# Kernel optimization log

Measured on AMD Instinct MI355X. Metric: run time of the kernel, lower is better.

Reference implementation:

```python
import jax, jax.numpy as jnp
import numpy as np

SEG = 512        # seg_len
REUSE = 2        # reuse_seg_num
D = 512          # d_model
K = 512          # k_dim
NL = 6           # layers per encoder
NSEG = 8         # number of segments (context 4096)
VOCAB = 10000
FF = 2048
MEM = REUSE * SEG


def sinusoid_pos_encode(length, dim):
    pos = jnp.arange(length, dtype=jnp.float32)[:, None]
    idx = jnp.arange(0, dim, 2, dtype=jnp.float32)
    ang = pos / jnp.power(10000.0, idx / dim)
    pe = jnp.zeros((length, dim), dtype=jnp.float32)
    pe = pe.at[:, 0::2].set(jnp.sin(ang))
    pe = pe.at[:, 1::2].set(jnp.cos(ang))
    return pe


def layernorm(x, g, b, eps=1e-5):
    mu = jnp.mean(x, axis=-1, keepdims=True)
    var = jnp.mean(jnp.square(x - mu), axis=-1, keepdims=True)
    return (x - mu) * jax.lax.rsqrt(var + eps) * g + b


def run_encoder(tokens, emb, Wqkvr, Wo, W1, W2, ln, uv):
    # tokens: (NSEG*SEG,) int
    segs = tokens.reshape(NSEG, SEG)
    R = jnp.flip(sinusoid_pos_encode(MEM + SEG, K), axis=0)  # flipped rel. encoding
    u, v = uv[0], uv[1]                                       # (K,), (K,)
    scale = 1.0 / np.sqrt(K)

    def step(prev, xs):
        seg, seg_idx = xs
        state = emb[seg]                                      # (SEG, D)
        # memory validity mask: only the last min(seg_idx, REUSE) segments are real
        n_valid = jnp.minimum(seg_idx, REUSE) * SEG
        mem_bias = jnp.where(jnp.arange(MEM) >= MEM - n_valid, 0.0, -1e9)
        bias = jnp.concatenate([mem_bias, jnp.zeros(SEG)])    # (MEM+SEG,)
        recs = []
        for j in range(NL):
            recs.append(state)
            mem = prev[:, j].reshape(MEM, D)                  # (MEM, D)
            Wq, Wk, Wv, Wr = Wqkvr[j]                         # each (D, K)
            q = state @ Wq                                    # (SEG, K)
            full = jnp.concatenate([mem, state], axis=0)      # (MEM+SEG, D)
            k = full @ Wk
            val = full @ Wv
            pk = R @ Wr                                       # (MEM+SEG, K)
            scores = ((q + u) @ k.T + (q + v) @ pk.T) * scale + bias[None, :]
            attn = jax.nn.softmax(scores, axis=-1)            # (SEG, MEM+SEG)
            out = (attn @ val) @ Wo[j]                        # (SEG, D)
            h = layernorm(state + out, ln[j, 0], ln[j, 1])
            ff = jax.nn.relu(h @ W1[j]) @ W2[j]
            state = layernorm(h + ff, ln[j, 2], ln[j, 3])
        # shift memory: drop oldest, append pre-layer states of this segment
        prev_new = jnp.concatenate([prev[1:], jnp.stack(recs)[None]], axis=0)
        return prev_new, state

    prev0 = jnp.zeros((REUSE, NL, SEG, D), dtype=jnp.float32)
    _, outs = jax.lax.scan(step, prev0, (segs, jnp.arange(NSEG)))
    return outs.reshape(-1, D)  # (NSEG*SEG, D)


def setup_inputs() -> dict:
    key = jax.random.key(0)
    ks = jax.random.split(key, 16)
    s = 0.02
    def mk(k, shape):
        return jax.random.normal(k, shape, dtype=jnp.float32) * s
    inp = {
        "src": jax.random.randint(ks[0], (1, NSEG * SEG), 0, VOCAB, dtype=jnp.int32),
        "pad_idx": 0,
        "emb": mk(ks[1], (VOCAB, D)),
        "Wqkvr_a": mk(ks[2], (NL, 4, D, K)),
        "Wo_a": mk(ks[3], (NL, K, D)),
        "W1_a": mk(ks[4], (NL, D, FF)),
        "W2_a": mk(ks[5], (NL, FF, D)),
        "ln_a": jnp.tile(jnp.array([1.0, 0.0, 1.0, 0.0], dtype=jnp.float32)[None, :, None], (NL, 1, D)),
        "uv_a": jax.random.normal(ks[6], (2, K), dtype=jnp.float32),
        "Wqkvr_b": mk(ks[7], (NL, 4, D, K)),
        "Wo_b": mk(ks[8], (NL, K, D)),
        "W1_b": mk(ks[9], (NL, D, FF)),
        "W2_b": mk(ks[10], (NL, FF, D)),
        "ln_b": jnp.tile(jnp.array([1.0, 0.0, 1.0, 0.0], dtype=jnp.float32)[None, :, None], (NL, 1, D)),
        "uv_b": jax.random.normal(ks[11], (2, K), dtype=jnp.float32),
    }
    return inp


def reference(src, pad_idx, emb, Wqkvr_a, Wo_a, W1_a, W2_a, ln_a, uv_a,
              Wqkvr_b, Wo_b, W1_b, W2_b, ln_b, uv_b):
    tokens = src[0]
    fwd = run_encoder(tokens, emb, Wqkvr_a, Wo_a, W1_a, W2_a, ln_a, uv_a)
    rev = run_encoder(tokens[::-1], emb, Wqkvr_b, Wo_b, W1_b, W2_b, ln_b, uv_b)
    rev = rev[::-1]
    return jnp.concatenate([fwd, rev], axis=-1)  # (NSEG*SEG, 2*D)
```

## Files before the change

kernel.cpp:

```cpp
#include <hip/hip_runtime.h>

typedef __bf16 bf16;
typedef __bf16 bf16x8 __attribute__((ext_vector_type(8)));
typedef __bf16 bf16x4 __attribute__((ext_vector_type(4)));
typedef __bf16 bf16x2 __attribute__((ext_vector_type(2)));
typedef float f32x4 __attribute__((ext_vector_type(4)));

typedef __attribute__((address_space(3))) void lds_void_t;
typedef const __attribute__((address_space(1))) void gbl_void_t;

#define TOK 4096
#define KBROWS 5120

enum { M_BF16 = 0, M_F32 = 1, M_RELU = 2, M_QKV = 3, M_SCOREXP = 4, M_PV = 5 };

struct GemmArgs {
  const bf16* A; long long sAe, sAi; int ldA;
  const bf16* B; long long sBe, sBi; int ldB;
  const bf16* B2; long long sB2e; int ldB2;
  bf16* C; float* Cf; long long sCe, sCi; int ldC;
  int M, N, K, iPerE;
  bf16 *quv, *kbuf, *vt;
  const float *uvA, *uvB;
  float scale;
};

template<int MODE, bool SPLITB, int TM, int TN>
__global__ __launch_bounds__(256, 4)
void gemm_kernel(GemmArgs g) {
  constexpr int FA = TM / 32, FB = TN / 32;
  int z = blockIdx.z;
  int e = z / g.iPerE;
  int i = z % g.iPerE;
  const bf16* A = g.A + e * g.sAe + i * g.sAi;
  const bf16* B = g.B + e * g.sBe + i * g.sBi;
  const bf16* B2 = nullptr;
  if constexpr (SPLITB) B2 = g.B2 + e * g.sB2e;

  int tm = blockIdx.x * TM;
  int tn = blockIdx.y * TN;

  __shared__ uint4 As4[TM * 8];
  __shared__ uint4 Bs4[TN * 8];
  __shared__ float ls[MODE == M_PV ? TM : 1];
  bf16* As_lds = (bf16*)As4;
  bf16* Bs_lds = (bf16*)Bs4;

  int tid = threadIdx.x;
  int wave = tid >> 6, lane = tid & 63;
  int wm = (wave >> 1) * (TM / 2), wn = (wave & 1) * (TN / 2);
  int quad = lane >> 4, l15 = lane & 15;
  int l7 = l15 & 7;
  int l8r = lane >> 3, l8c = lane & 7;
  int fc = l8c ^ l8r;

  f32x4 acc[FA][FB] = {};
  float lreg[FA];
#pragma unroll
  for (int t = 0; t < FA; ++t) lreg[t] = 0.f;

  for (int k0 = 0; k0 < g.K; k0 += 64) {
#pragma unroll
    for (int ii = 0; ii < FA; ++ii) {
      int rowbase = (wave * FA + ii) * 8;
      int r = rowbase + l8r;
      const bf16* gp = &A[(long long)(tm + r) * g.ldA + k0 + fc * 8];
      __builtin_amdgcn_global_load_lds((gbl_void_t*)gp, (lds_void_t*)&As_lds[rowbase * 64], 16, 0, 0);
    }
#pragma unroll
    for (int ii = 0; ii < FB; ++ii) {
      int rowbase = (wave * FB + ii) * 8;
      int r = rowbase + l8r;
      const bf16* gp;
      if constexpr (SPLITB) {
        int kk = k0 + fc * 8;
        gp = (kk < 512) ? &B[(long long)(tn + r) * g.ldB + kk]
                        : &B2[(long long)(tn + r) * g.ldB2 + (kk - 512)];
      } else {
        gp = &B[(long long)(tn + r) * g.ldB + k0 + fc * 8];
      }
      __builtin_amdgcn_global_load_lds((gbl_void_t*)gp, (lds_void_t*)&Bs_lds[rowbase * 64], 16, 0, 0);
    }
    __syncthreads();
#pragma unroll
    for (int s = 0; s < 2; ++s) {
      int sw = (s * 4 + quad) ^ l7;
      bf16x8 af[FA], bfr[FB];
#pragma unroll
      for (int t = 0; t < FA; ++t) af[t]  = ((const bf16x8*)As4)[(wm + t * 16 + l15) * 8 + sw];
#pragma unroll
      for (int t = 0; t < FB; ++t) bfr[t] = ((const bf16x8*)Bs4)[(wn + t * 16 + l15) * 8 + sw];
      if constexpr (MODE == M_PV) {
#pragma unroll
        for (int t = 0; t < FA; ++t)
#pragma unroll
          for (int q2 = 0; q2 < 8; ++q2) lreg[t] += (float)af[t][q2];
      }
#pragma unroll
      for (int a = 0; a < FA; ++a)
#pragma unroll
        for (int b = 0; b < FB; ++b)
          acc[a][b] = __builtin_amdgcn_mfma_f32_16x16x32_bf16(af[a], bfr[b], acc[a][b], 0, 0, 0);
    }
    __syncthreads();
  }

  if constexpr (MODE == M_PV) {
#pragma unroll
    for (int t = 0; t < FA; ++t) {
      lreg[t] += __shfl_xor(lreg[t], 16);
      lreg[t] += __shfl_xor(lreg[t], 32);
      if (quad == 0) ls[wm + t * 16 + l15] = lreg[t];
    }
    __syncthreads();
  }

  if constexpr (MODE == M_QKV) {
    const float* uv = e ? g.uvB : g.uvA;
#pragma unroll
    for (int a = 0; a < FA; ++a) {
      int mB = tm + wm + a * 16 + quad * 4;
#pragma unroll
      for (int b = 0; b < FB; ++b) {
        int col = tn + wn + b * 16 + l15;
        int region = col >> 9, cin = col & 511;
        float u0 = 0.f, v0 = 0.f;
        if (region == 0) { u0 = uv[cin]; v0 = uv[512 + cin]; }
#pragma unroll
        for (int r = 0; r < 4; ++r) {
          int m = mB + r;
          float val = acc[a][b][r];
          if (region == 0) {
            long long qb = (long long)e * TOK * 1024 + (long long)m * 1024;
            g.quv[qb + cin]       = (bf16)(val + u0);
            g.quv[qb + 512 + cin] = (bf16)(val + v0);
          } else if (region == 1) {
            g.kbuf[(long long)e * KBROWS * 512 + (long long)(1024 + m) * 512 + cin] = (bf16)val;
          } else {
            g.vt[(long long)e * 512 * KBROWS + (long long)cin * KBROWS + 1024 + m] = (bf16)val;
          }
        }
      }
    }
  } else if constexpr (MODE == M_SCOREXP) {
    bf16* C = g.C + e * g.sCe + i * g.sCi;
    int T = 1024 - ((i < 2 ? i : 2) << 9);
#pragma unroll
    for (int a = 0; a < FA; ++a) {
      int mB = tm + wm + a * 16 + quad * 4;
#pragma unroll
      for (int b = 0; b < FB; ++b) {
        int col = tn + wn + b * 16 + l15;
        float bias = (col < T) ? -1e9f : 0.0f;
#pragma unroll
        for (int r = 0; r < 4; ++r)
          C[(long long)(mB + r) * g.ldC + col] = (bf16)__expf(acc[a][b][r] * g.scale + bias);
      }
    }
  } else if constexpr (MODE == M_PV) {
    float* Cf = g.Cf + e * g.sCe + i * g.sCi;
#pragma unroll
    for (int a = 0; a < FA; ++a) {
      int lrow = wm + a * 16 + quad * 4;
      int mB = tm + lrow;
#pragma unroll
      for (int b = 0; b < FB; ++b) {
        int col = tn + wn + b * 16 + l15;
#pragma unroll
        for (int r = 0; r < 4; ++r)
          Cf[(long long)(mB + r) * g.ldC + col] = acc[a][b][r] / ls[lrow + r];
      }
    }
  } else {
#pragma unroll
    for (int a = 0; a < FA; ++a) {
      int mB = tm + wm + a * 16 + quad * 4;
#pragma unroll
      for (int b = 0; b < FB; ++b) {
        int col = tn + wn + b * 16 + l15;
#pragma unroll
        for (int r = 0; r < 4; ++r) {
          float val = acc[a][b][r];
          if constexpr (MODE == M_RELU) val = val > 0.f ? val : 0.f;
          if constexpr (MODE == M_F32) {
            float* Cf = g.Cf + e * g.sCe + i * g.sCi;
            Cf[(long long)(mB + r) * g.ldC + col] = val;
          } else {
            bf16* C = g.C + e * g.sCe + i * g.sCi;
            C[(long long)(mB + r) * g.ldC + col] = (bf16)val;
          }
        }
      }
    }
  }
}

__device__ inline void prep_locate(int id, const float* qa, const float* qb,
                                   const float* oa, const float* ob,
                                   const float* w1a, const float* w1b,
                                   const float* w2a, const float* w2b,
                                   bf16* wqkvT, bf16* wrT, bf16* wvPlain, bf16* woT,
                                   bf16* w1T, bf16* w2T,
                                   const float*& src, bf16*& dst, int& R, int& C,
                                   int& tx, int& ty, bool& plain) {
  plain = false;
  if (id < 3072) {
    int mat = id >> 6, tile = id & 63;
    tx = tile & 7; ty = tile >> 3;
    int e = mat / 24, rj = mat % 24, j = rj >> 2, c = rj & 3;
    src = (e ? qb : qa) + (long long)(j * 4 + c) * 262144;
    R = 512; C = 512;
    if (c < 2)        dst = wqkvT + ((long long)(e * 6 + j) * 3 + c) * 262144;
    else if (c == 2) { dst = wvPlain + (long long)(e * 6 + j) * 262144; plain = true; }
    else              dst = wrT + (long long)(e * 6 + j) * 262144;
  } else if (id < 3840) {
    int id2 = id - 3072; int mat = id2 >> 6, tile = id2 & 63;
    tx = tile & 7; ty = tile >> 3;
    int e = mat / 6, j = mat % 6;
    src = (e ? ob : oa) + (long long)j * 262144;
    dst = woT + (long long)mat * 262144; R = 512; C = 512;
  } else if (id < 6912) {
    int id2 = id - 3840; int mat = id2 >> 8, tile = id2 & 255;
    tx = tile & 31; ty = tile >> 5;
    int e = mat / 6, j = mat % 6;
    src = (e ? w1b : w1a) + (long long)j * 512 * 2048;
    dst = w1T + (long long)mat * 512 * 2048; R = 512; C = 2048;
  } else {
    int id2 = id - 6912; int mat = id2 >> 8, tile = id2 & 255;
    tx = tile & 7; ty = tile >> 3;
    int e = mat / 6, j = mat % 6;
    src = (e ? w2b : w2a) + (long long)j * 2048 * 512;
    dst = w2T + (long long)mat * 2048 * 512; R = 2048; C = 512;
  }
}

__global__ __launch_bounds__(256)
void prep_weights(const float* qa, const float* qb, const float* oa, const float* ob,
                  const float* w1a, const float* w1b, const float* w2a, const float* w2b,
                  bf16* wqkvT, bf16* wrT, bf16* wvPlain, bf16* woT, bf16* w1T, bf16* w2T) {
  int id0 = blockIdx.x * 2;
  const float* src; bf16* dst; int R, C, tx0, ty; bool plain;
  prep_locate(id0, qa, qb, oa, ob, w1a, w1b, w2a, w2b,
              wqkvT, wrT, wvPlain, woT, w1T, w2T, src, dst, R, C, tx0, ty, plain);
  int r0 = ty * 64;
  int tid = threadIdx.x;

  if (plain) {
    int c8 = (tid & 7) * 8;
    int r8 = tid >> 3;
    float4 f[2][4];
#pragma unroll
    for (int p = 0; p < 2; ++p) {
      int c0 = (tx0 + p) * 64;
#pragma unroll
      for (int rep = 0; rep < 2; ++rep) {
        const float* sp = &src[(long long)(r0 + r8 + rep * 32) * C + c0 + c8];
        f[p][rep * 2]     = *(const float4*)sp;
        f[p][rep * 2 + 1] = *(const float4*)(sp + 4);
      }
    }
#pragma unroll
    for (int p = 0; p < 2; ++p) {
      int c0 = (tx0 + p) * 64;
#pragma unroll
      for (int rep = 0; rep < 2; ++rep) {
        float4 f0 = f[p][rep * 2], f1 = f[p][rep * 2 + 1];
        bf16 o[8] __attribute__((aligned(16))) =
          {(bf16)f0.x, (bf16)f0.y, (bf16)f0.z, (bf16)f0.w,
           (bf16)f1.x, (bf16)f1.y, (bf16)f1.z, (bf16)f1.w};
        *(bf16x8*)&dst[(long long)(r0 + r8 + rep * 32) * C + c0 + c8] = *(const bf16x8*)o;
      }
    }
  } else {
    __shared__ bf16 t[2][64 * 68];
    int l15 = tid & 15;
    int hi  = tid >> 4;
    int cc = l15 * 4;
    float4 f[2][4];
#pragma unroll
    for (int p = 0; p < 2; ++p) {
      int c0 = (tx0 + p) * 64;
#pragma unroll
      for (int rep = 0; rep < 4; ++rep)
        f[p][rep] = *(const float4*)&src[(long long)(r0 + hi + rep * 16) * C + c0 + cc];
    }
#pragma unroll
    for (int p = 0; p < 2; ++p)
#pragma unroll
      for (int rep = 0; rep < 4; ++rep) {
        int rr = hi + rep * 16;
        float v[4] = {f[p][rep].x, f[p][rep].y, f[p][rep].z, f[p][rep].w};
#pragma unroll
        for (int i2 = 0; i2 < 4; ++i2) {
          int row = cc + i2;
          int col = rr ^ (((row >> 4) & 3) << 2);
          t[p][row * 68 + col] = (bf16)v[i2];
        }
      }
    __syncthreads();
    int oc = tid >> 2;
    int kk = tid & 3;
#pragma unroll
    for (int p = 0; p < 2; ++p) {
      int c0 = (tx0 + p) * 64;
      bf16 outv[16] __attribute__((aligned(16)));
#pragma unroll
      for (int u = 0; u < 4; ++u) {
        int col = (16 * kk + 4 * u) ^ (((oc >> 4) & 3) << 2);
        *(bf16x4*)&outv[u * 4] = *(const bf16x4*)&t[p][oc * 68 + col];
      }
      bf16* dp = &dst[(long long)(c0 + oc) * R + r0 + 16 * kk];
      *(bf16x8*)dp       = *(const bf16x8*)&outv[0];
      *(bf16x8*)(dp + 8) = *(const bf16x8*)&outv[8];
    }
  }
}

__global__ __launch_bounds__(256)
void sinusoid_kernel(bf16* rb) {
  int i = blockIdx.x, m = threadIdx.x;
  float p = (float)(1535 - i);
  float inv = expf(-((float)(2 * m) * (1.0f / 512.0f)) * 9.210340371976184f);
  float ang = p * inv;
  bf16x2 v = {(bf16)sinf(ang), (bf16)cosf(ang)};
  *(bf16x2*)&rb[(long long)i * 512 + 2 * m] = v;
}

__global__ __launch_bounds__(128)
void embed_kernel(const int* src, const float* emb, bf16* Sb, float* Sf) {
  int row = blockIdx.x, e = blockIdx.y, tid = threadIdx.x;
  int tok = e ? src[4095 - row] : src[row];
  long long base = ((long long)e * TOK + row) * 512 + tid * 4;
  float4 f = *(const float4*)&emb[(long long)tok * 512 + tid * 4];
  *(float4*)&Sf[base] = f;
  bf16 o[4] __attribute__((aligned(8))) = {(bf16)f.x, (bf16)f.y, (bf16)f.z, (bf16)f.w};
  *(bf16x4*)&Sb[base] = *(const bf16x4*)o;
}

__global__ __launch_bounds__(256)
void zero_kv(bf16* kbuf, bf16* vwoT) {
  int r = blockIdx.x, e = blockIdx.y, which = blockIdx.z, tid = threadIdx.x;
  uint4 z = {0u, 0u, 0u, 0u};
  if (which == 0) {
    if (tid < 64) ((uint4*)(kbuf + ((long long)e * KBROWS + r) * 512))[tid] = z;
  } else if (r < 512) {
    if (tid < 128) ((uint4*)(vwoT + ((long long)e * 512 + r) * KBROWS))[tid] = z;
  }
}

__global__ __launch_bounds__(64)
void ln_kernel(const float* Xf, const float* Tf, const float* lnA, const float* lnB,
               int gOff, bf16* OutB, float* OutF, int outMode, float* finalOut) {
  int row = blockIdx.x, e = blockIdx.y;
  long long base = ((long long)e * TOK + row) * 512;
  const float* ln = e ? lnB : lnA;
  int lane = threadIdx.x;
  int d0 = lane * 8;
  float4 x0 = *(const float4*)&Xf[base + d0];
  float4 x1 = *(const float4*)&Xf[base + d0 + 4];
  float4 t0 = *(const float4*)&Tf[base + d0];
  float4 t1 = *(const float4*)&Tf[base + d0 + 4];
  float vals[8] = {x0.x + t0.x, x0.y + t0.y, x0.z + t0.z, x0.w + t0.w,
                   x1.x + t1.x, x1.y + t1.y, x1.z + t1.z, x1.w + t1.w};
  float s = 0.f;
#pragma unroll
  for (int k = 0; k < 8; ++k) s += vals[k];
  for (int off = 32; off; off >>= 1) s += __shfl_xor(s, off);
  float mu = s * (1.0f / 512.0f);
  float vs = 0.f;
#pragma unroll
  for (int k = 0; k < 8; ++k) { float d = vals[k] - mu; vs += d * d; }
  for (int off = 32; off; off >>= 1) vs += __shfl_xor(vs, off);
  float rstd = rsqrtf(vs * (1.0f / 512.0f) + 1e-5f);
  float4 g0 = *(const float4*)&ln[gOff + d0];
  float4 g1 = *(const float4*)&ln[gOff + d0 + 4];
  float4 b0 = *(const float4*)&ln[gOff + 512 + d0];
  float4 b1 = *(const float4*)&ln[gOff + 512 + d0 + 4];
  float gm[8] = {g0.x, g0.y, g0.z, g0.w, g1.x, g1.y, g1.z, g1.w};
  float bt[8] = {b0.x, b0.y, b0.z, b0.w, b1.x, b1.y, b1.z, b1.w};
  float y[8];
#pragma unroll
  for (int k = 0; k < 8; ++k) y[k] = (vals[k] - mu) * rstd * gm[k] + bt[k];
  if (outMode == 0) {
    bf16 ob8[8] __attribute__((aligned(16)));
#pragma unroll
    for (int k = 0; k < 8; ++k) ob8[k] = (bf16)y[k];
    *(bf16x8*)&OutB[base + d0] = *(const bf16x8*)ob8;
    float4 ya = {y[0], y[1], y[2], y[3]}, yb = {y[4], y[5], y[6], y[7]};
    *(float4*)&OutF[base + d0]     = ya;
    *(float4*)&OutF[base + d0 + 4] = yb;
  } else {
    long long ob = e ? ((long long)(4095 - row) * 1024 + 512) : ((long long)row * 1024);
    float4 ya = {y[0], y[1], y[2], y[3]}, yb = {y[4], y[5], y[6], y[7]};
    *(float4*)&finalOut[ob + d0]     = ya;
    *(float4*)&finalOut[ob + d0 + 4] = yb;
  }
}

extern "C" void kernel_launch(void* const* d_in, const int* in_sizes, int n_in,
                              void* d_out, int out_size, void* d_ws, size_t ws_size,
                              hipStream_t stream) {
  const int*   src   = (const int*)d_in[0];
  const float* emb   = (const float*)d_in[2];
  const float* Wq_a  = (const float*)d_in[3];
  const float* Wo_a  = (const float*)d_in[4];
  const float* W1_a  = (const float*)d_in[5];
  const float* W2_a  = (const float*)d_in[6];
  const float* ln_a  = (const float*)d_in[7];
  const float* uv_a  = (const float*)d_in[8];
  const float* Wq_b  = (const float*)d_in[9];
  const float* Wo_b  = (const float*)d_in[10];
  const float* W1_b  = (const float*)d_in[11];
  const float* W2_b  = (const float*)d_in[12];
  const float* ln_b  = (const float*)d_in[13];
  const float* uv_b  = (const float*)d_in[14];
  float* out = (float*)d_out;

  char* w = (char*)d_ws;
  size_t off = 0;
  auto alloc = [&](long long elems, int esz) -> char* {
    char* p = w + off;
    off += (size_t)elems * esz;
    off = (off + 255) & ~(size_t)255;
    return p;
  };
  bf16* wqkvT = (bf16*)alloc(2LL * 6 * 1536 * 512, 2);
  bf16* woT   = (bf16*)alloc(2LL * 6 * 512 * 512, 2);
  bf16* w1T   = (bf16*)alloc(2LL * 6 * 2048 * 512, 2);
  bf16* w2T   = (bf16*)alloc(2LL * 6 * 512 * 2048, 2);
  bf16* pk    = (bf16*)alloc(2LL * 6 * 1536 * 512, 2);
  bf16* Sb    = (bf16*)alloc(2LL * TOK * 512, 2);
  float* Sf   = (float*)alloc(2LL * TOK * 512, 4);
  bf16* quv   = (bf16*)alloc(2LL * TOK * 1024, 2);
  bf16* kbuf  = (bf16*)alloc(2LL * KBROWS * 512, 2);
  bf16* vwoT  = (bf16*)alloc(2LL * 512 * KBROWS, 2);
  bf16* P     = (bf16*)alloc(2LL * 8 * 512 * 1536, 2);
  float* t1f  = (float*)alloc(2LL * TOK * 512, 4);
  bf16* f1    = (bf16*)alloc(2LL * TOK * 2048, 2);
  bf16* rb      = f1;
  bf16* wrT     = f1 + 1024LL * 1024;
  bf16* wvPlain = f1 + 4096LL * 1024;

  if (off > ws_size) return;

  prep_weights<<<4992, 256, 0, stream>>>(Wq_a, Wq_b, Wo_a, Wo_b, W1_a, W1_b, W2_a, W2_b,
                                         wqkvT, wrT, wvPlain, woT, w1T, w2T);
  sinusoid_kernel<<<1536, 256, 0, stream>>>(rb);
  embed_kernel<<<dim3(4096, 2), 128, 0, stream>>>(src, emb, Sb, Sf);
  zero_kv<<<dim3(1024, 2, 2), 256, 0, stream>>>(kbuf, vwoT);

  {
    GemmArgs g = {};
    g.A = rb; g.sAe = 0; g.sAi = 0; g.ldA = 512;
    g.B = wrT; g.sBe = 0; g.sBi = 512LL * 512; g.ldB = 512;
    g.C = pk; g.sCe = 0; g.sCi = 1536LL * 512; g.ldC = 512;
    g.M = 1536; g.N = 512; g.K = 512; g.iPerE = 12;
    gemm_kernel<M_BF16, false, 128, 128><<<dim3(12, 4, 12), 256, 0, stream>>>(g);
  }
  {
    GemmArgs g = {};
    g.A = woT; g.sAe = 6LL * 262144; g.sAi = 262144; g.ldA = 512;
    g.B = wvPlain; g.sBe = 6LL * 262144; g.sBi = 262144; g.ldB = 512;
    g.C = wqkvT + 2LL * 262144; g.sCe = 18LL * 262144; g.sCi = 3LL * 262144; g.ldC = 512;
    g.M = 512; g.N = 512; g.K = 512; g.iPerE = 6;
    gemm_kernel<M_BF16, false, 128, 128><<<dim3(4, 4, 12), 256, 0, stream>>>(g);
  }

  const float scale = 0.044194173824159216f;

  for (int j = 0; j < 6; ++j) {
    {
      GemmArgs g = {};
      g.A = Sb; g.sAe = (long long)TOK * 512; g.sAi = 0; g.ldA = 512;
      g.B = wqkvT + (long long)j * 1536 * 512; g.sBe = 6LL * 1536 * 512; g.sBi = 0; g.ldB = 512;
      g.M = TOK; g.N = 1536; g.K = 512; g.iPerE = 1;
      g.quv = quv; g.kbuf = kbuf; g.vt = vwoT; g.uvA = uv_a; g.uvB = uv_b;
      gemm_kernel<M_QKV, false, 128, 128><<<dim3(32, 12, 2), 256, 0, stream>>>(g);
    }
    {
      GemmArgs g = {};
      g.A = quv; g.sAe = (long long)TOK * 1024; g.sAi = 512LL * 1024; g.ldA = 1024;
      g.B = kbuf; g.sBe = (long long)KBROWS * 512; g.sBi = 512LL * 512; g.ldB = 512;
      g.B2 = pk + (long long)j * 1536 * 512; g.sB2e = 6LL * 1536 * 512; g.ldB2 = 512;
      g.C = P; g.sCe = 8LL * 512 * 1536; g.sCi = 512LL * 1536; g.ldC = 1536;
      g.M = 512; g.N = 1536; g.K = 1024; g.iPerE = 8;
      g.scale = scale;
      gemm_kernel<M_SCOREXP, true, 128, 128><<<dim3(4, 12, 16), 256, 0, stream>>>(g);
    }
    {
      GemmArgs g = {};
      g.A = P; g.sAe = 8LL * 512 * 1536; g.sAi = 512LL * 1536; g.ldA = 1536;
      g.B = vwoT; g.sBe = 512LL * KBROWS; g.sBi = 512; g.ldB = KBROWS;
      g.Cf = t1f; g.sCe = (long long)TOK * 512; g.sCi = 512LL * 512; g.ldC = 512;
      g.M = 512; g.N = 512; g.K = 1536; g.iPerE = 8;
      gemm_kernel<M_PV, false, 64, 128><<<dim3(8, 4, 16), 256, 0, stream>>>(g);
    }
    ln_kernel<<<dim3(4096, 2), 64, 0, stream>>>(Sf, t1f, ln_a, ln_b, (j * 4 + 0) * 512, Sb, Sf, 0, out);
    {
      GemmArgs g = {};
      g.A = Sb; g.sAe = (long long)TOK * 512; g.sAi = 0; g.ldA = 512;
      g.B = w1T + (long long)j * 2048 * 512; g.sBe = 6LL * 2048 * 512; g.sBi = 0; g.ldB = 512;
      g.C = f1; g.sCe = (long long)TOK * 2048; g.sCi = 0; g.ldC = 2048;
      g.M = TOK; g.N = 2048; g.K = 512; g.iPerE = 1;
      gemm_kernel<M_RELU, false, 128, 128><<<dim3(32, 16, 2), 256, 0, stream>>>(g);
    }
    {
      GemmArgs g = {};
      g.A = f1; g.sAe = (long long)TOK * 2048; g.sAi = 0; g.ldA = 2048;
      g.B = w2T + (long long)j * 512 * 2048; g.sBe = 6LL * 512 * 2048; g.sBi = 0; g.ldB = 2048;
      g.Cf = t1f; g.sCe = (long long)TOK * 512; g.sCi = 0; g.ldC = 512;
      g.M = TOK; g.N = 512; g.K = 2048; g.iPerE = 1;
      gemm_kernel<M_F32, false, 64, 128><<<dim3(64, 4, 2), 256, 0, stream>>>(g);
    }
    ln_kernel<<<dim3(4096, 2), 64, 0, stream>>>(Sf, t1f, ln_a, ln_b, (j * 4 + 2) * 512, Sb, Sf,
                                                (j == 5) ? 1 : 0, out);
  }
}
```

Measured before the change: 1.275 ms.

## Fuse setup kernels into one launch and stage V-transpose stores through LDS

Merges weight prep, sinusoid generation, embedding lookup and KV zeroing into one setup kernel, with each weight-prep block now handling four tiles instead of two. In the QKV GEMM epilogue the region is resolved per tile rather than per element, and the V-transposed output is staged through shared memory so it is written with 16-byte coalesced stores instead of scattered 2-byte strided writes. This is meant to cut launch overhead and uncoalesced global writes. The cost is more register pressure in the prep path and extra LDS traffic and a barrier in the epilogue.

Result: faster. 1.243 ms (-2.5%).

```diff
diff --git a/kernel.cpp b/kernel.cpp
--- a/kernel.cpp
+++ b/kernel.cpp
@@ -40,8 +40,9 @@
   int tm = blockIdx.x * TM;
   int tn = blockIdx.y * TN;
 
-  __shared__ uint4 As4[TM * 8];
-  __shared__ uint4 Bs4[TN * 8];
+  __shared__ uint4 smem[TM * 8 + TN * 8];
+  uint4* As4 = smem;
+  uint4* Bs4 = smem + TM * 8;
   __shared__ float ls[MODE == M_PV ? TM : 1];
   bf16* As_lds = (bf16*)As4;
   bf16* Bs_lds = (bf16*)Bs4;
@@ -117,28 +118,61 @@
 
   if constexpr (MODE == M_QKV) {
     const float* uv = e ? g.uvB : g.uvA;
-#pragma unroll
-    for (int a = 0; a < FA; ++a) {
-      int mB = tm + wm + a * 16 + quad * 4;
-#pragma unroll
-      for (int b = 0; b < FB; ++b) {
-        int col = tn + wn + b * 16 + l15;
-        int region = col >> 9, cin = col & 511;
-        float u0 = 0.f, v0 = 0.f;
-        if (region == 0) { u0 = uv[cin]; v0 = uv[512 + cin]; }
-#pragma unroll
-        for (int r = 0; r < 4; ++r) {
-          int m = mB + r;
-          float val = acc[a][b][r];
-          if (region == 0) {
+    int region = tn >> 9;
+    if (region == 2) {
+      bf16* sm = (bf16*)smem;
+#pragma unroll
+      for (int a = 0; a < FA; ++a) {
+        int m_l = wm + a * 16 + quad * 4;
+#pragma unroll
+        for (int b = 0; b < FB; ++b) {
+          int c_l = wn + b * 16 + l15;
+          int mp = m_l ^ ((c_l & 15) << 3);
+          bf16 v4[4] __attribute__((aligned(8)));
+#pragma unroll
+          for (int r = 0; r < 4; ++r) v4[r] = (bf16)acc[a][b][r];
+          *(bf16x4*)&sm[c_l * 128 + mp] = *(const bf16x4*)v4;
+        }
+      }
+      __syncthreads();
+      int c_l = tid >> 1;
+      int half = (tid & 1) * 64;
+      long long vb = (long long)e * 512 * KBROWS + (long long)(tn - 1024 + c_l) * KBROWS + 1024 + tm;
+#pragma unroll
+      for (int u = 0; u < 8; ++u) {
+        int m0 = half + u * 8;
+        int mp = m0 ^ ((c_l & 15) << 3);
+        *(bf16x8*)&g.vt[vb + m0] = *(const bf16x8*)&sm[c_l * 128 + mp];
+      }
+    } else if (region == 0) {
+#pragma unroll
+      for (int a = 0; a < FA; ++a) {
+        int mB = tm + wm + a * 16 + quad * 4;
+#pragma unroll
+        for (int b = 0; b < FB; ++b) {
+          int cin = tn + wn + b * 16 + l15;
+          float u0 = uv[cin], v0 = uv[512 + cin];
+#pragma unroll
+          for (int r = 0; r < 4; ++r) {
+            int m = mB + r;
+            float val = acc[a][b][r];
             long long qb = (long long)e * TOK * 1024 + (long long)m * 1024;
             g.quv[qb + cin]       = (bf16)(val + u0);
             g.quv[qb + 512 + cin] = (bf16)(val + v0);
-          } else if (region == 1) {
-            g.kbuf[(long long)e * KBROWS * 512 + (long long)(1024 + m) * 512 + cin] = (bf16)val;
-          } else {
-            g.vt[(long long)e * 512 * KBROWS + (long long)cin * KBROWS + 1024 + m] = (bf16)val;
           }
+        }
+      }
+    } else {
+#pragma unroll
+      for (int a = 0; a < FA; ++a) {
+        int mB = tm + wm + a * 16 + quad * 4;
+#pragma unroll
+        for (int b = 0; b < FB; ++b) {
+          int cin = (tn - 512) + wn + b * 16 + l15;
+#pragma unroll
+          for (int r = 0; r < 4; ++r)
+            g.kbuf[(long long)e * KBROWS * 512 + (long long)(1024 + mB + r) * 512 + cin] =
+                (bf16)acc[a][b][r];
         }
       }
     }
@@ -235,116 +269,151 @@
 }
 
 __global__ __launch_bounds__(256)
-void prep_weights(const float* qa, const float* qb, const float* oa, const float* ob,
+void setup_kernel(const float* qa, const float* qb, const float* oa, const float* ob,
                   const float* w1a, const float* w1b, const float* w2a, const float* w2b,
-                  bf16* wqkvT, bf16* wrT, bf16* wvPlain, bf16* woT, bf16* w1T, bf16* w2T) {
-  int id0 = blockIdx.x * 2;
-  const float* src; bf16* dst; int R, C, tx0, ty; bool plain;
-  prep_locate(id0, qa, qb, oa, ob, w1a, w1b, w2a, w2b,
-              wqkvT, wrT, wvPlain, woT, w1T, w2T, src, dst, R, C, tx0, ty, plain);
-  int r0 = ty * 64;
+                  bf16* wqkvT, bf16* wrT, bf16* wvPlain, bf16* woT, bf16* w1T, bf16* w2T,
+                  bf16* rb, const int* src, const float* emb, bf16* Sb, float* Sf,
+                  bf16* kbuf, bf16* vwoT) {
+  __shared__ bf16 t[2][64 * 68];
+  int bid = blockIdx.x;
   int tid = threadIdx.x;
 
-  if (plain) {
-    int c8 = (tid & 7) * 8;
-    int r8 = tid >> 3;
-    float4 f[2][4];
-#pragma unroll
-    for (int p = 0; p < 2; ++p) {
-      int c0 = (tx0 + p) * 64;
-#pragma unroll
-      for (int rep = 0; rep < 2; ++rep) {
-        const float* sp = &src[(long long)(r0 + r8 + rep * 32) * C + c0 + c8];
-        f[p][rep * 2]     = *(const float4*)sp;
-        f[p][rep * 2 + 1] = *(const float4*)(sp + 4);
-      }
-    }
-#pragma unroll
-    for (int p = 0; p < 2; ++p) {
-      int c0 = (tx0 + p) * 64;
-#pragma unroll
-      for (int rep = 0; rep < 2; ++rep) {
-        float4 f0 = f[p][rep * 2], f1 = f[p][rep * 2 + 1];
-        bf16 o[8] __attribute__((aligned(16))) =
-          {(bf16)f0.x, (bf16)f0.y, (bf16)f0.z, (bf16)f0.w,
-           (bf16)f1.x, (bf16)f1.y, (bf16)f1.z, (bf16)f1.w};
-        *(bf16x8*)&dst[(long long)(r0 + r8 + rep * 32) * C + c0 + c8] = *(const bf16x8*)o;
-      }
-    }
+  if (bid < 2496) {
+    int id0 = bid * 4;
+    const float* src_w; bf16* dst; int R, C, tx0, ty; bool plain;
+    prep_locate(id0, qa, qb, oa, ob, w1a, w1b, w2a, w2b,
+                wqkvT, wrT, wvPlain, woT, w1T, w2T, src_w, dst, R, C, tx0, ty, plain);
+    int r0 = ty * 64;
+
+    if (plain) {
+      int c8 = (tid & 7) * 8;
+      int r8 = tid >> 3;
+      float4 f[4][4];
+#pragma unroll
+      for (int p = 0; p < 4; ++p) {
+        int c0 = (tx0 + p) * 64;
+#pragma unroll
+        for (int rep = 0; rep < 2; ++rep) {
+          const float* sp = &src_w[(long long)(r0 + r8 + rep * 32) * C + c0 + c8];
+          f[p][rep * 2]     = *(const float4*)sp;
+          f[p][rep * 2 + 1] = *(const float4*)(sp + 4);
+        }
+      }
+#pragma unroll
+      for (int p = 0; p < 4; ++p) {
+        int c0 = (tx0 + p) * 64;
+#pragma unroll
+        for (int rep = 0; rep < 2; ++rep) {
+          float4 f0 = f[p][rep * 2], f1 = f[p][rep * 2 + 1];
+          bf16 o[8] __attribute__((aligned(16))) =
+            {(bf16)f0.x, (bf16)f0.y, (bf16)f0.z, (bf16)f0.w,
+             (bf16)f1.x, (bf16)f1.y, (bf16)f1.z, (bf16)f1.w};
+          *(bf16x8*)&dst[(long long)(r0 + r8 + rep * 32) * C + c0 + c8] = *(const bf16x8*)o;
+        }
+      }
+    } else {
+      int l15 = tid & 15;
+      int hi  = tid >> 4;
+      int cc = l15 * 4;
+      int oc = tid >> 2;
+      int kk = tid & 3;
+      float4 fA[2][4], fB[2][4];
+#pragma unroll
+      for (int p = 0; p < 2; ++p) {
+        int c0 = (tx0 + p) * 64;
+#pragma unroll
+        for (int rep = 0; rep < 4; ++rep)
+          fA[p][rep] = *(const float4*)&src_w[(long long)(r0 + hi + rep * 16) * C + c0 + cc];
+      }
+#pragma unroll
+      for (int p = 0; p < 2; ++p)
+#pragma unroll
+        for (int rep = 0; rep < 4; ++rep) {
+          int rr = hi + rep * 16;
+          float v[4] = {fA[p][rep].x, fA[p][rep].y, fA[p][rep].z, fA[p][rep].w};
+#pragma unroll
+          for (int i2 = 0; i2 < 4; ++i2) {
+            int row = cc + i2;
+            int col = rr ^ (((row >> 4) & 3) << 2);
+            t[p][row * 68 + col] = (bf16)v[i2];
+          }
+        }
+#pragma unroll
+      for (int p = 0; p < 2; ++p) {
+        int c0 = (tx0 + 2 + p) * 64;
+#pragma unroll
+        for (int rep = 0; rep < 4; ++rep)
+          fB[p][rep] = *(const float4*)&src_w[(long long)(r0 + hi + rep * 16) * C + c0 + cc];
+      }
+      __syncthreads();
+#pragma unroll
+      for (int p = 0; p < 2; ++p) {
+        int c0 = (tx0 + p) * 64;
+        bf16 outv[16] __attribute__((aligned(16)));
+#pragma unroll
+        for (int u = 0; u < 4; ++u) {
+          int col = (16 * kk + 4 * u) ^ (((oc >> 4) & 3) << 2);
+          *(bf16x4*)&outv[u * 4] = *(const bf16x4*)&t[p][oc * 68 + col];
+        }
+        bf16* dp = &dst[(long long)(c0 + oc) * R + r0 + 16 * kk];
+        *(bf16x8*)dp       = *(const bf16x8*)&outv[0];
+        *(bf16x8*)(dp + 8) = *(const bf16x8*)&outv[8];
+      }
+      __syncthreads();
+#pragma unroll
+      for (int p = 0; p < 2; ++p)
+#pragma unroll
+        for (int rep = 0; rep < 4; ++rep) {
+          int rr = hi + rep * 16;
+          float v[4] = {fB[p][rep].x, fB[p][rep].y, fB[p][rep].z, fB[p][rep].w};
+#pragma unroll
+          for (int i2 = 0; i2 < 4; ++i2) {
+            int row = cc + i2;
+            int col = rr ^ (((row >> 4) & 3) << 2);
+            t[p][row * 68 + col] = (bf16)v[i2];
+          }
+        }
+      __syncthreads();
+#pragma unroll
+      for (int p = 0; p < 2; ++p) {
+        int c0 = (tx0 + 2 + p) * 64;
+        bf16 outv[16] __attribute__((aligned(16)));
+#pragma unroll
+        for (int u = 0; u < 4; ++u) {
+          int col = (16 * kk + 4 * u) ^ (((oc >> 4) & 3) << 2);
+          *(bf16x4*)&outv[u * 4] = *(const bf16x4*)&t[p][oc * 68 + col];
+        }
+        bf16* dp = &dst[(long long)(c0 + oc) * R + r0 + 16 * kk];
+        *(bf16x8*)dp       = *(const bf16x8*)&outv[0];
+        *(bf16x8*)(dp + 8) = *(const bf16x8*)&outv[8];
+      }
+    }
+  } else if (bid < 4032) {
+    int i = bid - 2496, m = tid;
+    float p = (float)(1535 - i);
+    float inv = expf(-((float)(2 * m) * (1.0f / 512.0f)) * 9.210340371976184f);
+    float ang = p * inv;
+    bf16x2 v = {(bf16)sinf(ang), (bf16)cosf(ang)};
+    *(bf16x2*)&rb[(long long)i * 512 + 2 * m] = v;
+  } else if (bid < 8128) {
+    int rp = (bid - 4032) * 2 + (tid >> 7);
+    int e2 = rp >> 12, row = rp & 4095;
+    int t2 = tid & 127;
+    int tok = e2 ? src[4095 - row] : src[row];
+    long long base = ((long long)e2 * TOK + row) * 512 + t2 * 4;
+    float4 f = *(const float4*)&emb[(long long)tok * 512 + t2 * 4];
+    *(float4*)&Sf[base] = f;
+    bf16 o[4] __attribute__((aligned(8))) = {(bf16)f.x, (bf16)f.y, (bf16)f.z, (bf16)f.w};
+    *(bf16x4*)&Sb[base] = *(const bf16x4*)o;
   } else {
-    __shared__ bf16 t[2][64 * 68];
-    int l15 = tid & 15;
-    int hi  = tid >> 4;
-    int cc = l15 * 4;
-    float4 f[2][4];
-#pragma unroll
-    for (int p = 0; p < 2; ++p) {
-      int c0 = (tx0 + p) * 64;
-#pragma unroll
-      for (int rep = 0; rep < 4; ++rep)
-        f[p][rep] = *(const float4*)&src[(long long)(r0 + hi + rep * 16) * C + c0 + cc];
-    }
-#pragma unroll
-    for (int p = 0; p < 2; ++p)
-#pragma unroll
-      for (int rep = 0; rep < 4; ++rep) {
-        int rr = hi + rep * 16;
-        float v[4] = {f[p][rep].x, f[p][rep].y, f[p][rep].z, f[p][rep].w};
-#pragma unroll
-        for (int i2 = 0; i2 < 4; ++i2) {
-          int row = cc + i2;
-          int col = rr ^ (((row >> 4) & 3) << 2);
-          t[p][row * 68 + col] = (bf16)v[i2];
-        }
-      }
-    __syncthreads();
-    int oc = tid >> 2;
-    int kk = tid & 3;
-#pragma unroll
-    for (int p = 0; p < 2; ++p) {
-      int c0 = (tx0 + p) * 64;
-      bf16 outv[16] __attribute__((aligned(16)));
-#pragma unroll
-      for (int u = 0; u < 4; ++u) {
-        int col = (16 * kk + 4 * u) ^ (((oc >> 4) & 3) << 2);
-        *(bf16x4*)&outv[u * 4] = *(const bf16x4*)&t[p][oc * 68 + col];
-      }
-      bf16* dp = &dst[(long long)(c0 + oc) * R + r0 + 16 * kk];
-      *(bf16x8*)dp       = *(const bf16x8*)&outv[0];
-      *(bf16x8*)(dp + 8) = *(const bf16x8*)&outv[8];
-    }
-  }
-}
-
-__global__ __launch_bounds__(256)
-void sinusoid_kernel(bf16* rb) {
-  int i = blockIdx.x, m = threadIdx.x;
-  float p = (float)(1535 - i);
-  float inv = expf(-((float)(2 * m) * (1.0f / 512.0f)) * 9.210340371976184f);
-  float ang = p * inv;
-  bf16x2 v = {(bf16)sinf(ang), (bf16)cosf(ang)};
-  *(bf16x2*)&rb[(long long)i * 512 + 2 * m] = v;
-}
-
-__global__ __launch_bounds__(128)
-void embed_kernel(const int* src, const float* emb, bf16* Sb, float* Sf) {
-  int row = blockIdx.x, e = blockIdx.y, tid = threadIdx.x;
-  int tok = e ? src[4095 - row] : src[row];
-  long long base = ((long long)e * TOK + row) * 512 + tid * 4;
-  float4 f = *(const float4*)&emb[(long long)tok * 512 + tid * 4];
-  *(float4*)&Sf[base] = f;
-  bf16 o[4] __attribute__((aligned(8))) = {(bf16)f.x, (bf16)f.y, (bf16)f.z, (bf16)f.w};
-  *(bf16x4*)&Sb[base] = *(const bf16x4*)o;
-}
-
-__global__ __launch_bounds__(256)
-void zero_kv(bf16* kbuf, bf16* vwoT) {
-  int r = blockIdx.x, e = blockIdx.y, which = blockIdx.z, tid = threadIdx.x;
-  uint4 z = {0u, 0u, 0u, 0u};
-  if (which == 0) {
-    if (tid < 64) ((uint4*)(kbuf + ((long long)e * KBROWS + r) * 512))[tid] = z;
-  } else if (r < 512) {
-    if (tid < 128) ((uint4*)(vwoT + ((long long)e * 512 + r) * KBROWS))[tid] = z;
+    int idx = bid - 8128;
+    int which = idx >> 11, e2 = (idx >> 10) & 1, r = idx & 1023;
+    uint4 zv = {0u, 0u, 0u, 0u};
+    if (which == 0) {
+      if (tid < 64) ((uint4*)(kbuf + ((long long)e2 * KBROWS + r) * 512))[tid] = zv;
+    } else if (r < 512) {
+      if (tid < 128) ((uint4*)(vwoT + ((long long)e2 * 512 + r) * KBROWS))[tid] = zv;
+    }
   }
 }
 
@@ -443,11 +512,9 @@
 
   if (off > ws_size) return;
 
-  prep_weights<<<4992, 256, 0, stream>>>(Wq_a, Wq_b, Wo_a, Wo_b, W1_a, W1_b, W2_a, W2_b,
-                                         wqkvT, wrT, wvPlain, woT, w1T, w2T);
-  sinusoid_kernel<<<1536, 256, 0, stream>>>(rb);
-  embed_kernel<<<dim3(4096, 2), 128, 0, stream>>>(src, emb, Sb, Sf);
-  zero_kv<<<dim3(1024, 2, 2), 256, 0, stream>>>(kbuf, vwoT);
+  setup_kernel<<<12224, 256, 0, stream>>>(Wq_a, Wq_b, Wo_a, Wo_b, W1_a, W1_b, W2_a, W2_b,
+                                          wqkvT, wrT, wvPlain, woT, w1T, w2T,
+                                          rb, src, emb, Sb, Sf, kbuf, vwoT);
 
   {
     GemmArgs g = {};
```
